# Optimization experiments

Hardware: AMD Instinct MI355X
Metric: run time of the kernel (lower is better)

Reference implementation:

```python
import jax, jax.numpy as jnp
import numpy as np

B, T, CIN, H, W = 1, 8, 32, 256, 256
CO, NH, WS = 64, 8, 8  # C_out, n_head, wind_size


def conv3x3(x, w, b):
    # x: [N, C, h, w], w: [O, I, 3, 3], stride 1, padding 1 (SAME for 3x3)
    y = jax.lax.conv_general_dilated(
        x, w, window_strides=(1, 1), padding=((1, 1), (1, 1)),
        dimension_numbers=("NCHW", "OIHW", "NCHW"))
    return y + b[None, :, None, None]


def setup_inputs() -> dict:
    key = jax.random.key(0)
    ks = jax.random.split(key, 9)
    s = 0.05  # small init scale keeps attention logits well-conditioned
    f32 = jnp.float32
    return {
        "x": jax.random.normal(ks[0], (B, T, CIN, H, W), f32),
        "Wq": jax.random.normal(ks[1], (CO, CIN, 3, 3), f32) * s,
        "bq": jax.random.normal(ks[2], (CO,), f32) * s,
        "Wk": jax.random.normal(ks[3], (CO, CIN, 3, 3), f32) * s,
        "bk": jax.random.normal(ks[4], (CO,), f32) * s,
        "Wv": jax.random.normal(ks[5], (CO, CIN, 3, 3), f32) * s,
        "bv": jax.random.normal(ks[6], (CO,), f32) * s,
        "Wo": jax.random.normal(ks[7], (CO, CO, 3, 3), f32) * s,
        "bo": jax.random.normal(ks[8], (CO,), f32) * s,
    }


def reference(x, Wq, bq, Wk, bk, Wv, bv, Wo, bo):
    b, t, c, h, w = x.shape
    Hg, Wg = h // WS, w // WS          # grid of windows
    hc = CO // NH                      # per-head channels
    d = hc * WS * WS                   # per-window token dim

    # im2grid: [B,T,C,H,W] -> [B*T*Hg*Wg, C, Ws, Ws] (each window a conv batch elem)
    xg = (x.reshape(b, t, c, Hg, WS, Wg, WS)
           .transpose(0, 1, 3, 5, 2, 4, 6)
           .reshape(b * t * Hg * Wg, c, WS, WS))

    def proj(wgt, bias):
        y = conv3x3(xg, wgt, bias)                        # [BTHWg, CO, Ws, Ws]
        y = y.reshape(b, t, Hg * Wg, NH, hc, WS, WS)      # split heads (nh outer in channel)
        return y.transpose(0, 1, 3, 2, 4, 5, 6).reshape(b, t, NH, Hg * Wg, d)

    q, k, v = proj(Wq, bq), proj(Wk, bk), proj(Wv, bv)    # [B,T,nh,HWg,d]

    att = jnp.einsum("btnqd,btnkd->btnqk", q, k) * (1.0 / np.sqrt(d)).astype(x.dtype)
    att = jax.nn.softmax(att, axis=-1)                    # [B,T,nh,HWg,HWg]
    y = jnp.einsum("btnqk,btnkd->btnqd", att, v)          # [B,T,nh,HWg,d]

    # back to image: [B,T,nh,HWg,hc,Ws,Ws] -> [B,T,CO,Hg,Wg,Ws,Ws] -> [B,T,CO,H,W]
    y = (y.reshape(b, t, NH, Hg * Wg, hc, WS, WS)
          .transpose(0, 1, 2, 4, 3, 5, 6)
          .reshape(b, t, CO, Hg, Wg, WS, WS)
          .transpose(0, 1, 2, 3, 5, 4, 6)
          .reshape(b, t, CO, h, w))

    out = y + conv3x3(y.reshape(b * t, CO, h, w), Wo, bo).reshape(b, t, CO, h, w)
    return out
```

## Files before the change

kernel.cpp:

```cpp
#include <hip/hip_runtime.h>
#include <hip/hip_bf16.h>
#include <stdint.h>


using bf16 = __hip_bfloat16;
typedef short bf16x8 __attribute__((ext_vector_type(8)));
typedef short bf16x4 __attribute__((ext_vector_type(4)));
typedef float f32x4 __attribute__((ext_vector_type(4)));

#define AS1 __attribute__((address_space(1)))
#define AS3 __attribute__((address_space(3)))

__device__ __forceinline__ void gload_lds16(const void* g, void* l) {
  __builtin_amdgcn_global_load_lds((const AS1 unsigned int*)g, (AS3 unsigned int*)l, 16, 0, 0);
}
__device__ __forceinline__ float b2f(unsigned short u) {
  union { unsigned int i; float f; } x; x.i = ((unsigned)u) << 16; return x.f;
}
__device__ __forceinline__ unsigned short f2b(float f) {
  __hip_bfloat16 h = __float2bfloat16(f);
  return *reinterpret_cast<unsigned short*>(&h);
}

__global__ __launch_bounds__(256) void prep_w(const float* __restrict__ Wq, const float* __restrict__ Wk,
                                              const float* __restrict__ Wv, const float* __restrict__ Wo,
                                              bf16* __restrict__ wt, bf16* __restrict__ wot) {
  int i = blockIdx.x * 256 + threadIdx.x;
  if (i < 9 * 192 * 32) {
    int ci = i & 31, co192 = (i >> 5) % 192, s = i / 6144;
    int dy = s / 3, dx = s % 3;
    int proj = co192 >> 6, co = co192 & 63;
    const float* Ws = (proj == 0) ? Wq : ((proj == 1) ? Wk : Wv);
    wt[i] = __float2bfloat16(Ws[((co * 32 + ci) * 3 + dy) * 3 + dx]);
  }
  if (i < 9 * 64 * 64) {
    int ci = i & 63, co = (i >> 6) & 63, s = i >> 12;
    wot[i] = __float2bfloat16(Wo[((co * 64 + ci) * 3 + (s / 3)) * 3 + (s % 3)]);
  }
}

__global__ __launch_bounds__(256) void qkv_conv(const float* __restrict__ x, const bf16* __restrict__ wt,
                                                const float* __restrict__ bq, const float* __restrict__ bk,
                                                const float* __restrict__ bv,
                                                bf16* __restrict__ qout, bf16* __restrict__ kout,
                                                bf16* __restrict__ vout) {
  __shared__ bf16 xp[8000];
  int tid = threadIdx.x, bid = blockIdx.x;
  int t = bid >> 9, g = bid & 511;
  int gy = g >> 4, gx0 = (g & 15) * 2;

  unsigned int* xp32 = (unsigned int*)xp;
  for (int i = tid; i < 4000; i += 256) xp32[i] = 0u;
  __syncthreads();
  const float* xb = x + (size_t)t * 32 * 65536;
  #pragma unroll
  for (int it = 0; it < 16; ++it) {
    int e = tid + it * 256;
    int ix = e & 7, win = (e >> 3) & 1, iy = (e >> 4) & 7, ci = e >> 7;
    float val = xb[(size_t)ci * 65536 + (gy * 8 + iy) * 256 + (gx0 + win) * 8 + ix];
    xp[(win * 100 + (iy + 1) * 10 + (ix + 1)) * 40 + ci] = __float2bfloat16(val);
  }
  __syncthreads();

  int wv = tid >> 6, l = tid & 63, l15 = l & 15, lg = l >> 4;
  f32x4 z4 = {0.f, 0.f, 0.f, 0.f};
  f32x4 acc[3][8];
  for (int i = 0; i < 3; ++i) for (int j = 0; j < 8; ++j) acc[i][j] = z4;

  #pragma unroll
  for (int s = 0; s < 9; ++s) {
    const int dy = s / 3, dx = s % 3;
    bf16x8 a[3];
    #pragma unroll
    for (int mt = 0; mt < 3; ++mt)
      a[mt] = *(const bf16x8*)&wt[((size_t)s * 192 + wv * 48 + mt * 16 + l15) * 32 + lg * 8];
    #pragma unroll
    for (int nt = 0; nt < 8; ++nt) {
      int n = nt * 16 + l15;
      int win = n >> 6, px = n & 63;
      int iy = px >> 3, ix = px & 7;
      bf16x8 b = *(const bf16x8*)&xp[(win * 100 + (iy + dy) * 10 + (ix + dx)) * 40 + lg * 8];
      #pragma unroll
      for (int mt = 0; mt < 3; ++mt)
        acc[mt][nt] = __builtin_amdgcn_mfma_f32_16x16x32_bf16(a[mt], b, acc[mt][nt], 0, 0, 0);
    }
  }

  #pragma unroll
  for (int mt = 0; mt < 3; ++mt) {
    int c0 = wv * 48 + mt * 16 + lg * 4;
    int proj = c0 >> 6;
    int co0 = c0 & 63;
    int head = co0 >> 3, jj0 = co0 & 7;
    const float* bptr = (proj == 0) ? bq : ((proj == 1) ? bk : bv);
    bf16* dst = (proj == 0) ? qout : ((proj == 1) ? kout : vout);
    float bias[4];
    #pragma unroll
    for (int r = 0; r < 4; ++r) bias[r] = bptr[co0 + r];
    size_t bh = (size_t)(t * 8 + head);
    #pragma unroll
    for (int nt = 0; nt < 8; ++nt) {
      int n = nt * 16 + l15;
      int win2 = n >> 6, pyix = n & 63;
      size_t gwin = (size_t)gy * 32 + gx0 + win2;
      bf16x4 pack;
      #pragma unroll
      for (int r = 0; r < 4; ++r) pack[r] = (short)f2b(acc[mt][nt][r] + bias[r]);
      *(bf16x4*)&dst[(bh * 1024 + gwin) * 512 + pyix * 8 + jj0] = pack;
    }
  }
}

__global__ __launch_bounds__(256) void transpose_v(const bf16* __restrict__ v, bf16* __restrict__ vt) {
  __shared__ bf16 tl[64 * 72];
  int tid = threadIdx.x, bid = blockIdx.x;
  int bh = bid >> 7, wtile = (bid >> 3) & 15, dtile = bid & 7;
  int w0 = wtile * 64, d0 = dtile * 64;
  const bf16* vb = v + ((size_t)bh * 1024 + w0) * 512 + d0;
  int win_l = tid >> 2, dseg = (tid & 3) * 16;
  bf16x8 x0 = *(const bf16x8*)&vb[(size_t)win_l * 512 + dseg];
  bf16x8 x1 = *(const bf16x8*)&vb[(size_t)win_l * 512 + dseg + 8];
  #pragma unroll
  for (int j = 0; j < 8; ++j) {
    *(short*)&tl[(dseg + j) * 72 + win_l] = x0[j];
    *(short*)&tl[(dseg + 8 + j) * 72 + win_l] = x1[j];
  }
  __syncthreads();
  int d_l = tid >> 2, wseg = (tid & 3) * 16;
  bf16x8 y0 = *(const bf16x8*)&tl[d_l * 72 + wseg];
  bf16x8 y1 = *(const bf16x8*)&tl[d_l * 72 + wseg + 8];
  bf16* vtb = vt + ((size_t)bh * 512 + d0 + d_l) * 1024 + w0 + wseg;
  *(bf16x8*)&vtb[0] = y0;
  *(bf16x8*)&vtb[8] = y1;
}

__device__ __forceinline__ void stage8(const bf16* __restrict__ Ab, const bf16* __restrict__ Bb,
                                       bf16* smem, int c, int t, int sk,
                                       int w, int lr, int sl) {
  #pragma unroll
  for (int p = 0; p < 4; ++p) {
    int row = p * 64 + w * 8 + lr;
    gload_lds16(Ab + (size_t)row * sk + t * 64 + sl * 8,
                (char*)smem + c * 65536 + p * 8192 + w * 1024);
    gload_lds16(Bb + (size_t)row * sk + t * 64 + sl * 8,
                (char*)smem + c * 65536 + 32768 + p * 8192 + w * 1024);
  }
}

__global__ __launch_bounds__(512, 2) void qk_gemm(const bf16* __restrict__ q, const bf16* __restrict__ k,
                                                  bf16* __restrict__ S) {
  __shared__ bf16 smem[65536];
  int tid = threadIdx.x;
  int bid = (blockIdx.x & 7) * 128 + (blockIdx.x >> 3);
  int batch = bid >> 4, tm = (bid >> 2) & 3, tn = bid & 3;
  const bf16* Qb = q + (size_t)batch * 1024 * 512 + (size_t)tm * 256 * 512;
  const bf16* Kb = k + (size_t)batch * 1024 * 512 + (size_t)tn * 256 * 512;
  int w = tid >> 6, l = tid & 63, l15 = l & 15, lg = l >> 4;
  int wm2 = w >> 2, wn4 = w & 3;
  int lr = l >> 3, sl = (l & 7) ^ lr, swz = l15 & 7;
  f32x4 z4 = {0.f, 0.f, 0.f, 0.f};
  f32x4 acc[8][4];
  for (int i = 0; i < 8; ++i) for (int j = 0; j < 4; ++j) acc[i][j] = z4;

  stage8(Qb, Kb, smem, 0, 0, 512, w, lr, sl);
  asm volatile("s_waitcnt vmcnt(0)" ::: "memory");
  __builtin_amdgcn_s_barrier();
  __builtin_amdgcn_sched_barrier(0);

  for (int t = 0; t < 8; ++t) {
    int c = t & 1;
    if (t + 1 < 8) stage8(Qb, Kb, smem, c ^ 1, t + 1, 512, w, lr, sl);
    const bf16* At = smem + c * 32768;
    const bf16* Bt = At + 16384;
    __builtin_amdgcn_s_setprio(1);
    #pragma unroll
    for (int kk = 0; kk < 2; ++kk) {
      int ps = (kk * 4 + lg) ^ swz;
      bf16x8 a[8], b[4];
      #pragma unroll
      for (int i = 0; i < 8; ++i)
        a[i] = *(const bf16x8*)&At[(wm2 * 128 + i * 16 + l15) * 64 + ps * 8];
      #pragma unroll
      for (int j = 0; j < 4; ++j)
        b[j] = *(const bf16x8*)&Bt[(wn4 * 64 + j * 16 + l15) * 64 + ps * 8];
      #pragma unroll
      for (int i = 0; i < 8; ++i)
        #pragma unroll
        for (int j = 0; j < 4; ++j)
          acc[i][j] = __builtin_amdgcn_mfma_f32_16x16x32_bf16(a[i], b[j], acc[i][j], 0, 0, 0);
    }
    __builtin_amdgcn_s_setprio(0);
    asm volatile("s_waitcnt vmcnt(0)" ::: "memory");
    __builtin_amdgcn_s_barrier();
    __builtin_amdgcn_sched_barrier(0);
  }

  const float SCALE = 0.04419417382415922f;
  bf16* Sb = S + (size_t)batch * 1024 * 1024;
  #pragma unroll
  for (int i = 0; i < 8; ++i)
    #pragma unroll
    for (int j = 0; j < 4; ++j)
      #pragma unroll
      for (int r = 0; r < 4; ++r) {
        int row = tm * 256 + wm2 * 128 + i * 16 + lg * 4 + r;
        int col = tn * 256 + wn4 * 64 + j * 16 + l15;
        Sb[(size_t)row * 1024 + col] = __float2bfloat16(acc[i][j][r] * SCALE);
      }
}

__global__ __launch_bounds__(256) void row_stats(const bf16* __restrict__ S, float2* __restrict__ pstats) {
  int l = threadIdx.x & 63;
  size_t row = (size_t)blockIdx.x * 4 + (threadIdx.x >> 6);
  const bf16* p = S + row * 1024 + l * 16;
  bf16x8 s0 = *(const bf16x8*)p;
  bf16x8 s1 = *(const bf16x8*)(p + 8);
  float f[16];
  #pragma unroll
  for (int i = 0; i < 8; ++i) { f[i] = b2f((unsigned short)s0[i]); f[8 + i] = b2f((unsigned short)s1[i]); }
  float m = f[0];
  #pragma unroll
  for (int i = 1; i < 16; ++i) m = fmaxf(m, f[i]);
  for (int d = 1; d < 64; d <<= 1) m = fmaxf(m, __shfl_xor(m, d));
  float sum = 0.f;
  #pragma unroll
  for (int i = 0; i < 16; ++i) sum += __expf(f[i] - m);
  for (int d = 1; d < 64; d <<= 1) sum += __shfl_xor(sum, d);
  if (l == 0) {
    float2 st; st.x = m; st.y = 1.0f / sum;
    pstats[row] = st;
  }
}

__global__ __launch_bounds__(512, 2) void pv_gemm(const bf16* __restrict__ S, const bf16* __restrict__ vt,
                                                  const float2* __restrict__ pstats,
                                                  bf16* __restrict__ y) {
  __shared__ bf16 smem[65536];
  int tid = threadIdx.x;
  int bid = (blockIdx.x & 7) * 64 + (blockIdx.x >> 3);
  int batch = bid >> 3, bq = (bid >> 1) & 3, bd = bid & 1;
  const bf16* Pb = S + (size_t)batch * 1024 * 1024 + (size_t)bq * 256 * 1024;
  const bf16* Vb = vt + (size_t)batch * 512 * 1024 + (size_t)bd * 256 * 1024;
  int w = tid >> 6, l = tid & 63, l15 = l & 15, lg = l >> 4;
  int wm2 = w >> 2, wn4 = w & 3;
  int lr = l >> 3, sl = (l & 7) ^ lr, swz = l15 & 7;
  f32x4 z4 = {0.f, 0.f, 0.f, 0.f};
  f32x4 acc[8][4];
  for (int i = 0; i < 8; ++i) for (int j = 0; j < 4; ++j) acc[i][j] = z4;

  float m4[4], r4[4];
  #pragma unroll
  for (int p = 0; p < 4; ++p) {
    float2 st = pstats[(size_t)batch * 1024 + bq * 256 + p * 64 + w * 8 + lr];
    m4[p] = st.x; r4[p] = st.y;
  }

  bf16x8 areg[4];
  #define PV_ISSUE(tt, cc)                                                        \
    {                                                                             \
      _Pragma("unroll")                                                           \
      for (int p = 0; p < 4; ++p)                                                 \
        areg[p] = *(const bf16x8*)&Pb[(size_t)(p * 64 + w * 8 + lr) * 1024 +      \
                                      (tt) * 64 + sl * 8];                        \
      _Pragma("unroll")                                                           \
      for (int p = 0; p < 4; ++p)                                                 \
        gload_lds16(Vb + (size_t)(p * 64 + w * 8 + lr) * 1024 + (tt) * 64 + sl * 8, \
                    (char*)smem + (cc) * 65536 + 32768 + p * 8192 + w * 1024);    \
    }
  #define PV_WRITE_A(cc)                                                          \
    {                                                                             \
      _Pragma("unroll")                                                           \
      for (int p = 0; p < 4; ++p) {                                               \
        bf16x8 o;                                                                 \
        _Pragma("unroll")                                                         \
        for (int e = 0; e < 8; ++e) {                                             \
          float fv = b2f((unsigned short)areg[p][e]);                             \
          o[e] = (short)f2b(__expf(fv - m4[p]) * r4[p]);                          \
        }                                                                         \
        *(bf16x8*)((char*)smem + (cc) * 65536 + p * 8192 + w * 1024 + l * 16) = o; \
      }                                                                           \
    }

  PV_ISSUE(0, 0);
  asm volatile("s_waitcnt vmcnt(0)" ::: "memory");
  PV_WRITE_A(0);
  asm volatile("s_waitcnt lgkmcnt(0)" ::: "memory");
  __builtin_amdgcn_s_barrier();
  __builtin_amdgcn_sched_barrier(0);

  for (int t = 0; t < 16; ++t) {
    int c = t & 1;
    if (t + 1 < 16) PV_ISSUE(t + 1, c ^ 1);
    const bf16* At = smem + c * 32768;
    const bf16* Bt = At + 16384;
    __builtin_amdgcn_s_setprio(1);
    #pragma unroll
    for (int kk = 0; kk < 2; ++kk) {
      int ps = (kk * 4 + lg) ^ swz;
      bf16x8 a[8], b[4];
      #pragma unroll
      for (int i = 0; i < 8; ++i)
        a[i] = *(const bf16x8*)&At[(wm2 * 128 + i * 16 + l15) * 64 + ps * 8];
      #pragma unroll
      for (int j = 0; j < 4; ++j)
        b[j] = *(const bf16x8*)&Bt[(wn4 * 64 + j * 16 + l15) * 64 + ps * 8];
      #pragma unroll
      for (int i = 0; i < 8; ++i)
        #pragma unroll
        for (int j = 0; j < 4; ++j)
          acc[i][j] = __builtin_amdgcn_mfma_f32_16x16x32_bf16(a[i], b[j], acc[i][j], 0, 0, 0);
    }
    __builtin_amdgcn_s_setprio(0);
    asm volatile("s_waitcnt vmcnt(0)" ::: "memory");
    if (t + 1 < 16) PV_WRITE_A(c ^ 1);
    asm volatile("s_waitcnt lgkmcnt(0)" ::: "memory");
    __builtin_amdgcn_s_barrier();
    __builtin_amdgcn_sched_barrier(0);
  }

  int t2 = batch >> 3, h = batch & 7;
  #pragma unroll
  for (int i = 0; i < 8; ++i)
    #pragma unroll
    for (int j = 0; j < 4; ++j)
      #pragma unroll
      for (int r = 0; r < 4; ++r) {
        int win = bq * 256 + wm2 * 128 + i * 16 + lg * 4 + r;
        int dp = bd * 256 + wn4 * 64 + j * 16 + l15;
        int jj = dp & 7, pyix = dp >> 3;
        int gy = win >> 5, gx = win & 31;
        int Y = gy * 8 + (pyix >> 3), X = gx * 8 + (pyix & 7);
        y[(((size_t)t2 * 256 + Y) * 256 + X) * 64 + h * 8 + jj] = __float2bfloat16(acc[i][j][r]);
      }
}

__global__ __launch_bounds__(256, 4) void out_conv(const bf16* __restrict__ yimg, const bf16* __restrict__ wot,
                                                   const float* __restrict__ bo, float* __restrict__ out) {
  __shared__ bf16 yp[324 * 76];
  int tid = threadIdx.x, bid = blockIdx.x;
  int t = bid >> 8, tile = bid & 255;
  int y0 = (tile >> 4) * 16, x0 = (tile & 15) * 16;
  const bf16* yb = yimg + (size_t)t * 256 * 256 * 64;

  for (int e = tid; e < 324 * 8; e += 256) {
    int seg = e & 7, pos = e >> 3;
    int ppx = pos % 18, ppy = pos / 18;
    int gy = y0 + ppy - 1, gx = x0 + ppx - 1;
    bf16x8 val = {0, 0, 0, 0, 0, 0, 0, 0};
    if ((unsigned)gy < 256u && (unsigned)gx < 256u)
      val = *(const bf16x8*)&yb[((size_t)gy * 256 + gx) * 64 + seg * 8];
    *(bf16x8*)&yp[pos * 76 + seg * 8] = val;
  }
  __syncthreads();

  int wv = tid >> 6, l = tid & 63, l15 = l & 15, lg = l >> 4;
  int wm = wv & 1, wn = wv >> 1;
  f32x4 z4 = {0.f, 0.f, 0.f, 0.f};
  f32x4 acc[2][8];
  for (int i = 0; i < 2; ++i) for (int j = 0; j < 8; ++j) acc[i][j] = z4;

  #pragma unroll
  for (int s9 = 0; s9 < 9; ++s9) {
    const int dy = s9 / 3, dx = s9 % 3;
    #pragma unroll
    for (int half = 0; half < 2; ++half) {
      bf16x8 a[2];
      #pragma unroll
      for (int mt = 0; mt < 2; ++mt)
        a[mt] = *(const bf16x8*)&wot[((size_t)s9 * 64 + wm * 32 + mt * 16 + l15) * 64 + half * 32 + lg * 8];
      #pragma unroll
      for (int nt = 0; nt < 8; ++nt) {
        int ty = wn * 8 + nt;
        bf16x8 b = *(const bf16x8*)&yp[((ty + dy) * 18 + l15 + dx) * 76 + half * 32 + lg * 8];
        #pragma unroll
        for (int mt = 0; mt < 2; ++mt)
          acc[mt][nt] = __builtin_amdgcn_mfma_f32_16x16x32_bf16(a[mt], b, acc[mt][nt], 0, 0, 0);
      }
    }
  }

  float* ob = out + (size_t)t * 64 * 65536;
  float bias[2][4];
  #pragma unroll
  for (int mt = 0; mt < 2; ++mt)
    #pragma unroll
    for (int r = 0; r < 4; ++r) bias[mt][r] = bo[wm * 32 + mt * 16 + lg * 4 + r];
  #pragma unroll
  for (int mt = 0; mt < 2; ++mt)
    #pragma unroll
    for (int nt = 0; nt < 8; ++nt) {
      int ty = wn * 8 + nt;
      #pragma unroll
      for (int r = 0; r < 4; ++r) {
        int co = wm * 32 + mt * 16 + lg * 4 + r;
        float res = b2f(*(const unsigned short*)&yp[((ty + 1) * 18 + l15 + 1) * 76 + co]);
        ob[(size_t)co * 65536 + (size_t)(y0 + ty) * 256 + x0 + l15] = res + acc[mt][nt][r] + bias[mt][r];
      }
    }
}

extern "C" void kernel_launch(void* const* d_in, const int* in_sizes, int n_in,
                              void* d_out, int out_size, void* d_ws, size_t ws_size,
                              hipStream_t stream) {
  const float* x  = (const float*)d_in[0];
  const float* Wq = (const float*)d_in[1];
  const float* bq = (const float*)d_in[2];
  const float* Wk = (const float*)d_in[3];
  const float* bk = (const float*)d_in[4];
  const float* Wv = (const float*)d_in[5];
  const float* bv = (const float*)d_in[6];
  const float* Wo = (const float*)d_in[7];
  const float* bo = (const float*)d_in[8];
  float* out = (float*)d_out;

  char* ws = (char*)d_ws;
  bf16* wt  = (bf16*)(ws + 0);
  bf16* wot = (bf16*)(ws + 110592);
  bf16* q   = (bf16*)(ws + 262144);
  bf16* k   = (bf16*)(ws + 67371008);
  float2* pstats = (float2*)(ws + 67371008);
  bf16* S   = (bf16*)(ws + 134479872);
  bf16* vt  = (bf16*)(ws + 268697600);
  bf16* y   = (bf16*)(ws + 262144);
  bf16* v   = S;

  prep_w<<<216, 256, 0, stream>>>(Wq, Wk, Wv, Wo, wt, wot);
  qkv_conv<<<4096, 256, 0, stream>>>(x, wt, bq, bk, bv, q, k, v);
  transpose_v<<<8192, 256, 0, stream>>>(v, vt);
  qk_gemm<<<1024, 512, 0, stream>>>(q, k, S);
  row_stats<<<16384, 256, 0, stream>>>(S, pstats);
  pv_gemm<<<512, 512, 0, stream>>>(S, vt, pstats, y);
  out_conv<<<2048, 256, 0, stream>>>(y, wot, bo, out);
}
```

Baseline: 434.8 us.

## Triple-buffer B operand in attention GEMMs to prefetch two stages ahead

In both the QK and PV GEMM kernels, the B operand (K, or transposed V) now goes into a three-slot LDS ring and is prefetched two K-steps ahead, while A stays double-buffered. Waits use a partial vmcnt so the newest loads can stay in flight across the barrier, and the K loops are fully unrolled. This hides more global-memory latency, but LDS per block grows to 160KB, so occupancy falls to one 512-thread block per CU (launch bounds lowered to match). Separately, out_conv drops its min-blocks launch bound and reads the four residual bf16 values with one vector LDS load instead of four scalar loads.

```diff
diff --git a/kernel.cpp b/kernel.cpp
--- a/kernel.cpp
+++ b/kernel.cpp
@@ -134,22 +134,9 @@
   *(bf16x8*)&vtb[8] = y1;
 }
 
-__device__ __forceinline__ void stage8(const bf16* __restrict__ Ab, const bf16* __restrict__ Bb,
-                                       bf16* smem, int c, int t, int sk,
-                                       int w, int lr, int sl) {
-  #pragma unroll
-  for (int p = 0; p < 4; ++p) {
-    int row = p * 64 + w * 8 + lr;
-    gload_lds16(Ab + (size_t)row * sk + t * 64 + sl * 8,
-                (char*)smem + c * 65536 + p * 8192 + w * 1024);
-    gload_lds16(Bb + (size_t)row * sk + t * 64 + sl * 8,
-                (char*)smem + c * 65536 + 32768 + p * 8192 + w * 1024);
-  }
-}
-
-__global__ __launch_bounds__(512, 2) void qk_gemm(const bf16* __restrict__ q, const bf16* __restrict__ k,
+__global__ __launch_bounds__(512, 1) void qk_gemm(const bf16* __restrict__ q, const bf16* __restrict__ k,
                                                   bf16* __restrict__ S) {
-  __shared__ bf16 smem[65536];
+  __shared__ bf16 smem[81920];
   int tid = threadIdx.x;
   int bid = (blockIdx.x & 7) * 128 + (blockIdx.x >> 3);
   int batch = bid >> 4, tm = (bid >> 2) & 3, tn = bid & 3;
@@ -162,16 +149,32 @@
   f32x4 acc[8][4];
   for (int i = 0; i < 8; ++i) for (int j = 0; j < 4; ++j) acc[i][j] = z4;
 
-  stage8(Qb, Kb, smem, 0, 0, 512, w, lr, sl);
-  asm volatile("s_waitcnt vmcnt(0)" ::: "memory");
+  #define QK_STG_A(T)                                                            \
+    { char* base = (char*)smem + ((T) & 1) * 32768;                              \
+      _Pragma("unroll")                                                          \
+      for (int p = 0; p < 4; ++p) {                                              \
+        int row = p * 64 + w * 8 + lr;                                           \
+        gload_lds16(Qb + (size_t)row * 512 + (T) * 64 + sl * 8,                  \
+                    base + p * 8192 + w * 1024); } }
+  #define QK_STG_B(T)                                                            \
+    { char* base = (char*)smem + 65536 + ((T) % 3) * 32768;                      \
+      _Pragma("unroll")                                                          \
+      for (int p = 0; p < 4; ++p) {                                              \
+        int row = p * 64 + w * 8 + lr;                                           \
+        gload_lds16(Kb + (size_t)row * 512 + (T) * 64 + sl * 8,                  \
+                    base + p * 8192 + w * 1024); } }
+
+  QK_STG_B(0); QK_STG_A(0); QK_STG_B(1);
+  asm volatile("s_waitcnt vmcnt(4)" ::: "memory");
   __builtin_amdgcn_s_barrier();
   __builtin_amdgcn_sched_barrier(0);
 
+  #pragma unroll
   for (int t = 0; t < 8; ++t) {
-    int c = t & 1;
-    if (t + 1 < 8) stage8(Qb, Kb, smem, c ^ 1, t + 1, 512, w, lr, sl);
-    const bf16* At = smem + c * 32768;
-    const bf16* Bt = At + 16384;
+    if (t + 1 < 8) QK_STG_A(t + 1);
+    if (t + 2 < 8) QK_STG_B(t + 2);
+    const bf16* At = (const bf16*)((char*)smem + (t & 1) * 32768);
+    const bf16* Bt = (const bf16*)((char*)smem + 65536 + (t % 3) * 32768);
     __builtin_amdgcn_s_setprio(1);
     #pragma unroll
     for (int kk = 0; kk < 2; ++kk) {
@@ -190,10 +193,13 @@
           acc[i][j] = __builtin_amdgcn_mfma_f32_16x16x32_bf16(a[i], b[j], acc[i][j], 0, 0, 0);
     }
     __builtin_amdgcn_s_setprio(0);
-    asm volatile("s_waitcnt vmcnt(0)" ::: "memory");
+    if (t + 2 < 8)      { asm volatile("s_waitcnt vmcnt(4)" ::: "memory"); }
+    else if (t + 1 < 8) { asm volatile("s_waitcnt vmcnt(0)" ::: "memory"); }
     __builtin_amdgcn_s_barrier();
     __builtin_amdgcn_sched_barrier(0);
   }
+  #undef QK_STG_A
+  #undef QK_STG_B
 
   const float SCALE = 0.04419417382415922f;
   bf16* Sb = S + (size_t)batch * 1024 * 1024;
@@ -232,10 +238,10 @@
   }
 }
 
-__global__ __launch_bounds__(512, 2) void pv_gemm(const bf16* __restrict__ S, const bf16* __restrict__ vt,
+__global__ __launch_bounds__(512, 1) void pv_gemm(const bf16* __restrict__ S, const bf16* __restrict__ vt,
                                                   const float2* __restrict__ pstats,
                                                   bf16* __restrict__ y) {
-  __shared__ bf16 smem[65536];
+  __shared__ bf16 smem[81920];
   int tid = threadIdx.x;
   int bid = (blockIdx.x & 7) * 64 + (blockIdx.x >> 3);
   int batch = bid >> 3, bq = (bid >> 1) & 3, bd = bid & 1;
@@ -256,19 +262,20 @@
   }
 
   bf16x8 areg[4];
-  #define PV_ISSUE(tt, cc)                                                        \
-    {                                                                             \
-      _Pragma("unroll")                                                           \
+  #define PV_ISSUE_A(tt)                                                          \
+    { _Pragma("unroll")                                                           \
       for (int p = 0; p < 4; ++p)                                                 \
         areg[p] = *(const bf16x8*)&Pb[(size_t)(p * 64 + w * 8 + lr) * 1024 +      \
-                                      (tt) * 64 + sl * 8];                        \
+                                      (tt) * 64 + sl * 8]; }
+  #define PV_STG_B(T)                                                             \
+    { char* base = (char*)smem + 65536 + ((T) % 3) * 32768;                       \
       _Pragma("unroll")                                                           \
-      for (int p = 0; p < 4; ++p)                                                 \
-        gload_lds16(Vb + (size_t)(p * 64 + w * 8 + lr) * 1024 + (tt) * 64 + sl * 8, \
-                    (char*)smem + (cc) * 65536 + 32768 + p * 8192 + w * 1024);    \
-    }
-  #define PV_WRITE_A(cc)                                                          \
-    {                                                                             \
+      for (int p = 0; p < 4; ++p) {                                               \
+        int row = p * 64 + w * 8 + lr;                                            \
+        gload_lds16(Vb + (size_t)row * 1024 + (T) * 64 + sl * 8,                  \
+                    base + p * 8192 + w * 1024); } }
+  #define PV_WRITE_A(buf)                                                         \
+    { char* base = (char*)smem + (buf) * 32768;                                   \
       _Pragma("unroll")                                                           \
       for (int p = 0; p < 4; ++p) {                                               \
         bf16x8 o;                                                                 \
@@ -277,22 +284,22 @@
           float fv = b2f((unsigned short)areg[p][e]);                             \
           o[e] = (short)f2b(__expf(fv - m4[p]) * r4[p]);                          \
         }                                                                         \
-        *(bf16x8*)((char*)smem + (cc) * 65536 + p * 8192 + w * 1024 + l * 16) = o; \
-      }                                                                           \
-    }
-
-  PV_ISSUE(0, 0);
-  asm volatile("s_waitcnt vmcnt(0)" ::: "memory");
+        *(bf16x8*)(base + p * 8192 + w * 1024 + l * 16) = o; }                    \
+    }
+
+  PV_STG_B(0); PV_ISSUE_A(0); PV_STG_B(1);
+  asm volatile("s_waitcnt vmcnt(4)" ::: "memory");
   PV_WRITE_A(0);
   asm volatile("s_waitcnt lgkmcnt(0)" ::: "memory");
   __builtin_amdgcn_s_barrier();
   __builtin_amdgcn_sched_barrier(0);
 
+  #pragma unroll
   for (int t = 0; t < 16; ++t) {
-    int c = t & 1;
-    if (t + 1 < 16) PV_ISSUE(t + 1, c ^ 1);
-    const bf16* At = smem + c * 32768;
-    const bf16* Bt = At + 16384;
+    if (t + 1 < 16) PV_ISSUE_A(t + 1);
+    if (t + 2 < 16) PV_STG_B(t + 2);
+    const bf16* At = (const bf16*)((char*)smem + (t & 1) * 32768);
+    const bf16* Bt = (const bf16*)((char*)smem + 65536 + (t % 3) * 32768);
     __builtin_amdgcn_s_setprio(1);
     #pragma unroll
     for (int kk = 0; kk < 2; ++kk) {
@@ -311,12 +318,16 @@
           acc[i][j] = __builtin_amdgcn_mfma_f32_16x16x32_bf16(a[i], b[j], acc[i][j], 0, 0, 0);
     }
     __builtin_amdgcn_s_setprio(0);
-    asm volatile("s_waitcnt vmcnt(0)" ::: "memory");
-    if (t + 1 < 16) PV_WRITE_A(c ^ 1);
+    if (t + 2 < 16)      { asm volatile("s_waitcnt vmcnt(4)" ::: "memory"); }
+    else if (t + 1 < 16) { asm volatile("s_waitcnt vmcnt(0)" ::: "memory"); }
+    if (t + 1 < 16) PV_WRITE_A((t + 1) & 1);
     asm volatile("s_waitcnt lgkmcnt(0)" ::: "memory");
     __builtin_amdgcn_s_barrier();
     __builtin_amdgcn_sched_barrier(0);
   }
+  #undef PV_ISSUE_A
+  #undef PV_STG_B
+  #undef PV_WRITE_A
 
   int t2 = batch >> 3, h = batch & 7;
   #pragma unroll
@@ -334,8 +345,8 @@
       }
 }
 
-__global__ __launch_bounds__(256, 4) void out_conv(const bf16* __restrict__ yimg, const bf16* __restrict__ wot,
-                                                   const float* __restrict__ bo, float* __restrict__ out) {
+__global__ __launch_bounds__(256) void out_conv(const bf16* __restrict__ yimg, const bf16* __restrict__ wot,
+                                                const float* __restrict__ bo, float* __restrict__ out) {
   __shared__ bf16 yp[324 * 76];
   int tid = threadIdx.x, bid = blockIdx.x;
   int t = bid >> 8, tile = bid & 255;
@@ -390,10 +401,11 @@
     #pragma unroll
     for (int nt = 0; nt < 8; ++nt) {
       int ty = wn * 8 + nt;
+      bf16x4 resv = *(const bf16x4*)&yp[((ty + 1) * 18 + l15 + 1) * 76 + wm * 32 + mt * 16 + lg * 4];
       #pragma unroll
       for (int r = 0; r < 4; ++r) {
         int co = wm * 32 + mt * 16 + lg * 4 + r;
-        float res = b2f(*(const unsigned short*)&yp[((ty + 1) * 18 + l15 + 1) * 76 + co]);
+        float res = b2f((unsigned short)resv[r]);
         ob[(size_t)co * 65536 + (size_t)(y0 + ty) * 256 + x0 + l15] = res + acc[mt][nt][r] + bias[mt][r];
       }
     }
```

New measurement: 436.1 us. Within noise of the previous version (+0.3%).
